# Optimization experiments

Hardware: AMD Instinct MI355X
Metric: run time of the kernel (lower is better)

## Reference

```python
import jax, jax.numpy as jnp
import numpy as np

TAU = 0.1

def setup_inputs() -> dict:
    key = jax.random.key(0)
    kZ, k1, k2 = jax.random.split(key, 3)
    N, D = 8192, 128
    scale = 1.0 / np.sqrt(D)
    return {
        "Z": jax.random.normal(kZ, (N, D), dtype=jnp.float32),
        "W1": jax.random.normal(k1, (D, D), dtype=jnp.float32) * scale,
        "b1": jnp.zeros((D,), dtype=jnp.float32),
        "W2": jax.random.normal(k2, (D, D), dtype=jnp.float32) * scale,
        "b2": jnp.zeros((D,), dtype=jnp.float32),
    }

def reference(Z, W1, b1, W2, b2):
    # DiffusivityTransform: 2-layer MLP with ReLU (torch Linear: x @ W.T + b;
    # here W1/W2 are stored already transposed as [in, out])
    t = jax.nn.relu(Z @ W1 + b1) @ W2 + b2          # [N, D]
    sim = t @ t.T                                     # [N, N]
    S = jax.nn.softmax(sim, axis=1)                   # row-stochastic [N, N]
    Z_prop = S @ Z                                    # [N, D]
    return Z + TAU * (Z_prop - Z)
```

## Files before the change

### kernel.cpp

```cpp
#include <hip/hip_runtime.h>

typedef _Float16 half_t;
typedef _Float16 hx8 __attribute__((ext_vector_type(8)));
typedef _Float16 hx4 __attribute__((ext_vector_type(4)));
typedef float fx4 __attribute__((ext_vector_type(4)));

#define LOG2E 1.44269504088896f
#define TAU 0.1f
#define NSPLIT 8

__global__ __launch_bounds__(256) void prep_kernel(
    const float* __restrict__ W1, const float* __restrict__ W2,
    const float* __restrict__ Z,
    half_t* __restrict__ W1t, half_t* __restrict__ W2t,
    half_t* __restrict__ Zth)
{
  __shared__ float tile[32*132];
  const int bx = blockIdx.x;
  const int tid = threadIdx.x;
  if (bx < 8) {
    const float* W = (bx & 4) ? W2 : W1;
    half_t* Wt = (bx & 4) ? W2t : W1t;
    const int i0 = (bx & 3) * 32;
    const int r = tid >> 3, cb = tid & 7;
#pragma unroll
    for (int it=0; it<4; ++it) {
      int c4 = cb*4 + it*32;
      *(fx4*)(&tile[r*132 + c4]) = *(const fx4*)(W + (size_t)(i0+r)*128 + c4);
    }
    __syncthreads();
    const int o = tid >> 1, ih = (tid & 1)*16;
    hx8 v0, v1;
#pragma unroll
    for (int u=0;u<8;++u) v0[u] = (half_t)tile[(ih+u)*132 + o];
#pragma unroll
    for (int u=0;u<8;++u) v1[u] = (half_t)tile[(ih+8+u)*132 + o];
    *(hx8*)(Wt + (size_t)o*128 + i0 + ih)     = v0;
    *(hx8*)(Wt + (size_t)o*128 + i0 + ih + 8) = v1;
  } else {
    float* zt = tile;
    const int b = bx - 8;
    const int nb = b >> 2;
    const int db = b & 3;
#pragma unroll
    for (int i=0;i<2;++i) {
      int fid = i*256 + tid;
      int r = fid >> 3, c4 = (fid & 7) * 4;
      *(fx4*)(&zt[r*36 + c4]) = *(const fx4*)(Z + (size_t)(nb*64 + r)*128 + db*32 + c4);
    }
    __syncthreads();
    const int cr = tid >> 3, j = tid & 7, n0 = j*8;
    hx8 hv;
#pragma unroll
    for (int idx=0;idx<8;++idx) hv[idx] = (half_t)zt[(n0+idx)*36 + cr];
    *(hx8*)(Zth + (size_t)(db*32 + cr)*8192 + nb*64 + n0) = hv;
  }
}

__global__ __launch_bounds__(128) void mlp_kernel(
    const float* __restrict__ Z, const half_t* __restrict__ W1t,
    const float* __restrict__ b1, const half_t* __restrict__ W2t,
    const float* __restrict__ b2, half_t* __restrict__ T)
{
  __shared__ half_t Hs[2][16*136];
  const int tid = threadIdx.x;
  const int w = tid >> 6, lane = tid & 63;
  const int q = lane >> 4, c = lane & 15;
  const int wrow = blockIdx.x*32 + w*16;

  hx8 zb[4];
#pragma unroll
  for (int ks=0;ks<4;++ks) {
    fx4 a = *(const fx4*)(Z + (size_t)(wrow + c)*128 + ks*32 + q*8);
    fx4 b = *(const fx4*)(Z + (size_t)(wrow + c)*128 + ks*32 + q*8 + 4);
#pragma unroll
    for (int u=0;u<4;++u) { zb[ks][u] = (half_t)a[u]; zb[ks][4+u] = (half_t)b[u]; }
  }
  fx4 acc[8];
#pragma unroll
  for (int mt=0;mt<8;++mt) acc[mt] = (fx4){0.f,0.f,0.f,0.f};
#pragma unroll
  for (int mt=0;mt<8;++mt)
#pragma unroll
    for (int ks=0;ks<4;++ks) {
      hx8 aw = *(const hx8*)(W1t + (size_t)(mt*16 + c)*128 + ks*32 + q*8);
      acc[mt] = __builtin_amdgcn_mfma_f32_16x16x32_f16(aw, zb[ks], acc[mt], 0,0,0);
    }
#pragma unroll
  for (int mt=0;mt<8;++mt) {
    fx4 bias = *(const fx4*)(b1 + mt*16 + 4*q);
    hx4 hv;
#pragma unroll
    for (int i=0;i<4;++i) {
      float h = acc[mt][i] + bias[i];
      hv[i] = (half_t)(h > 0.f ? h : 0.f);
    }
    *(hx4*)(&Hs[w][c*136 + mt*16 + 4*q]) = hv;
  }

  hx8 hb[4];
#pragma unroll
  for (int ks=0;ks<4;++ks) hb[ks] = *(const hx8*)(&Hs[w][c*136 + ks*32 + q*8]);
#pragma unroll
  for (int mt=0;mt<8;++mt) acc[mt] = (fx4){0.f,0.f,0.f,0.f};
#pragma unroll
  for (int mt=0;mt<8;++mt)
#pragma unroll
    for (int ks=0;ks<4;++ks) {
      hx8 aw = *(const hx8*)(W2t + (size_t)(mt*16 + c)*128 + ks*32 + q*8);
      acc[mt] = __builtin_amdgcn_mfma_f32_16x16x32_f16(aw, hb[ks], acc[mt], 0,0,0);
    }
#pragma unroll
  for (int mt=0;mt<8;++mt) {
    fx4 bias = *(const fx4*)(b2 + mt*16 + 4*q);
    hx4 tv;
#pragma unroll
    for (int i=0;i<4;++i) tv[i] = (half_t)(acc[mt][i] + bias[i]);
    *(hx4*)(T + (size_t)(wrow + c)*128 + mt*16 + 4*q) = tv;
  }
}

__global__ __launch_bounds__(256,2) void flash_kernel(
    const half_t* __restrict__ T, const half_t* __restrict__ Zt,
    half_t* __restrict__ Pacc, float* __restrict__ Pm, float* __restrict__ Pl)
{
  __shared__ half_t Tbuf[2][16*512];
  __shared__ half_t Zbuf[2][16*512];
  const int tid = threadIdx.x;
  const int w = tid >> 6, lane = tid & 63;
  const int q = lane >> 4, c = lane & 15;
  const int bx = blockIdx.x;
  const int qb = bx >> 3, kh = bx & 7;
  const int wrow = qb*128 + w*32;
  const int sw = (c & 7) * 8;

  hx8 bq[2][4];
#pragma unroll
  for (int nt=0;nt<2;++nt)
#pragma unroll
    for (int ks=0;ks<4;++ks)
      bq[nt][ks] = *(const hx8*)(T + (size_t)(wrow + nt*16 + c)*128 + ks*32 + q*8);

  fx4 oacc[8][2];
#pragma unroll
  for (int mtd=0;mtd<8;++mtd)
#pragma unroll
    for (int nt=0;nt<2;++nt) oacc[mtd][nt] = (fx4){0.f,0.f,0.f,0.f};
  float m_run[2] = {-1e30f,-1e30f};
  float l_run[2] = {0.f,0.f};

  const int kbase = kh*1024;

  auto issue_loads = [&](int kt0, int b) {
    if (w < 2) {
#pragma unroll
      for (int i=0;i<8;++i) {
        int f = w*8 + i, mt = f >> 2, ks = f & 3;
        const half_t* gp = T + (size_t)(kt0 + mt*16 + c)*128 + ks*32 + q*8;
        half_t* lp = &Tbuf[b][f*512 + lane*8];
        __builtin_amdgcn_global_load_lds(
            (const __attribute__((address_space(1))) void*)gp,
            (__attribute__((address_space(3))) void*)lp, 16, 0, 0);
      }
    } else {
#pragma unroll
      for (int i=0;i<8;++i) {
        int f2 = (w-2)*8 + i, mtd = f2 >> 1, ks2 = f2 & 1;
        const half_t* gp = Zt + (size_t)(mtd*16 + c)*8192 + kt0 + ks2*32 + q*8;
        half_t* lp = &Zbuf[b][f2*512 + lane*8];
        __builtin_amdgcn_global_load_lds(
            (const __attribute__((address_space(1))) void*)gp,
            (__attribute__((address_space(3))) void*)lp, 16, 0, 0);
      }
    }
  };

  issue_loads(kbase, 0);

  for (int t=0;t<16;++t) {
    const int cur = t & 1;
    __syncthreads();
    half_t* Tcur = Tbuf[cur];
    half_t* Zcur = Zbuf[cur];
    half_t* Psw  = &Tbuf[cur][w*2048];

    fx4 sacc[4][2];
#pragma unroll
    for (int mt=0;mt<4;++mt)
#pragma unroll
      for (int nt=0;nt<2;++nt) sacc[mt][nt] = (fx4){0.f,0.f,0.f,0.f};
#pragma unroll
    for (int ks=0;ks<4;++ks)
#pragma unroll
      for (int mt=0;mt<4;++mt) {
        hx8 ak = *(const hx8*)(&Tcur[(mt*4+ks)*512 + lane*8]);
        sacc[mt][0] = __builtin_amdgcn_mfma_f32_16x16x32_f16(ak, bq[0][ks], sacc[mt][0], 0,0,0);
        sacc[mt][1] = __builtin_amdgcn_mfma_f32_16x16x32_f16(ak, bq[1][ks], sacc[mt][1], 0,0,0);
      }

    hx4 pk[2][4];
#pragma unroll
    for (int nt=0;nt<2;++nt) {
      float mx = -1e30f;
#pragma unroll
      for (int mt=0;mt<4;++mt)
#pragma unroll
        for (int i=0;i<4;++i) mx = fmaxf(mx, sacc[mt][nt][i]);
      mx = fmaxf(mx, __shfl_xor(mx, 16, 64));
      mx = fmaxf(mx, __shfl_xor(mx, 32, 64));
      float mnew = fmaxf(m_run[nt], mx);
      float alpha = __builtin_amdgcn_exp2f((m_run[nt]-mnew)*LOG2E);
      m_run[nt] = mnew;
      float nb = mnew*LOG2E;
      float rs = 0.f;
#pragma unroll
      for (int mt=0;mt<4;++mt) {
#pragma unroll
        for (int i=0;i<4;++i) {
          float p = __builtin_amdgcn_exp2f(sacc[mt][nt][i]*LOG2E - nb);
          rs += p;
          pk[nt][mt][i] = (half_t)p;
        }
      }
      rs += __shfl_xor(rs, 16, 64);
      rs += __shfl_xor(rs, 32, 64);
      l_run[nt] = l_run[nt]*alpha + rs;
#pragma unroll
      for (int mtd=0;mtd<8;++mtd)
#pragma unroll
        for (int i=0;i<4;++i) oacc[mtd][nt][i] *= alpha;
    }

    __syncthreads();
    if (t < 15) issue_loads(kbase + (t+1)*64, cur ^ 1);

#pragma unroll
    for (int nt=0;nt<2;++nt)
#pragma unroll
      for (int mt=0;mt<4;++mt)
        *(hx4*)(&Psw[(nt*16 + c)*64 + ((mt*16 + 4*q) ^ sw)]) = pk[nt][mt];

#pragma unroll
    for (int ks2=0;ks2<2;++ks2) {
      hx8 bp0 = *(const hx8*)(&Psw[(c     )*64 + ((ks2*32 + q*8) ^ sw)]);
      hx8 bp1 = *(const hx8*)(&Psw[(16 + c)*64 + ((ks2*32 + q*8) ^ sw)]);
#pragma unroll
      for (int mtd=0;mtd<8;++mtd) {
        hx8 az = *(const hx8*)(&Zcur[(mtd*2+ks2)*512 + lane*8]);
        oacc[mtd][0] = __builtin_amdgcn_mfma_f32_16x16x32_f16(az, bp0, oacc[mtd][0], 0,0,0);
        oacc[mtd][1] = __builtin_amdgcn_mfma_f32_16x16x32_f16(az, bp1, oacc[mtd][1], 0,0,0);
      }
    }
  }

#pragma unroll
  for (int nt=0;nt<2;++nt) {
    float inv = 1.0f / l_run[nt];
    const size_t rowg = (size_t)(bx*128 + w*32 + nt*16 + c);
#pragma unroll
    for (int mtd=0;mtd<8;++mtd) {
      hx4 ov;
#pragma unroll
      for (int i=0;i<4;++i) ov[i] = (half_t)(oacc[mtd][nt][i]*inv);
      *(hx4*)(Pacc + rowg*128 + mtd*16 + 4*q) = ov;
    }
    if (q == 0) {
      Pm[rowg] = m_run[nt];
      Pl[rowg] = l_run[nt];
    }
  }
}

__global__ __launch_bounds__(256) void merge_kernel(
    const float* __restrict__ Z, const half_t* __restrict__ Pacc,
    const float* __restrict__ Pm, const float* __restrict__ Pl,
    float* __restrict__ out)
{
  const int th = blockIdx.x*256 + threadIdx.x;
  const int r = th >> 5, cg = th & 31;
  const int qb = r >> 7, rr = r & 127;
  float mk[NSPLIT], lk[NSPLIT];
  float M = -1e30f;
#pragma unroll
  for (int k=0;k<NSPLIT;++k) {
    int p = qb*NSPLIT + k;
    mk[k] = Pm[p*128 + rr];
    lk[k] = Pl[p*128 + rr];
    M = fmaxf(M, mk[k]);
  }
  float L = 0.f, wk[NSPLIT];
#pragma unroll
  for (int k=0;k<NSPLIT;++k) { wk[k] = lk[k]*__builtin_amdgcn_exp2f((mk[k]-M)*LOG2E); L += wk[k]; }
  float o0=0.f,o1=0.f,o2=0.f,o3=0.f;
#pragma unroll
  for (int k=0;k<NSPLIT;++k) {
    int p = qb*NSPLIT + k;
    hx4 v = *(const hx4*)(Pacc + ((size_t)p*128 + rr)*128 + cg*4);
    o0 += wk[k]*(float)v[0]; o1 += wk[k]*(float)v[1];
    o2 += wk[k]*(float)v[2]; o3 += wk[k]*(float)v[3];
  }
  float invL = 1.0f / L;
  fx4 zv = *(const fx4*)(Z + (size_t)r*128 + cg*4);
  fx4 res;
  res[0] = (1.f-TAU)*zv[0] + TAU*o0*invL;
  res[1] = (1.f-TAU)*zv[1] + TAU*o1*invL;
  res[2] = (1.f-TAU)*zv[2] + TAU*o2*invL;
  res[3] = (1.f-TAU)*zv[3] + TAU*o3*invL;
  *(fx4*)(out + (size_t)r*128 + cg*4) = res;
}

extern "C" void kernel_launch(void* const* d_in, const int* in_sizes, int n_in,
                              void* d_out, int out_size, void* d_ws, size_t ws_size,
                              hipStream_t stream) {
  const float* Z  = (const float*)d_in[0];
  const float* W1 = (const float*)d_in[1];
  const float* b1 = (const float*)d_in[2];
  const float* W2 = (const float*)d_in[3];
  const float* b2 = (const float*)d_in[4];
  float* out = (float*)d_out;

  char* ws = (char*)d_ws;
  const size_t NBLK = 64 * NSPLIT;
  half_t* Thi  = (half_t*)(ws);
  half_t* Zth  = (half_t*)(ws + (size_t)2*1024*1024);
  half_t* Pacc = (half_t*)(ws + (size_t)4*1024*1024);
  float*  Pm   = (float*)(ws + (size_t)4*1024*1024 + NBLK*128*128*2);
  float*  Pl   = Pm + NBLK*128;
  half_t* W1t  = (half_t*)(ws + (size_t)4*1024*1024 + NBLK*128*128*2 + 2*NBLK*128*4);
  half_t* W2t  = W1t + 128*128;

  hipLaunchKernelGGL(prep_kernel,  dim3(520),  dim3(256), 0, stream, W1, W2, Z, W1t, W2t, Zth);
  hipLaunchKernelGGL(mlp_kernel,   dim3(256),  dim3(128), 0, stream, Z, W1t, b1, W2t, b2, Thi);
  hipLaunchKernelGGL(flash_kernel, dim3(NBLK), dim3(256), 0, stream, Thi, Zth, Pacc, Pm, Pl);
  hipLaunchKernelGGL(merge_kernel, dim3(1024), dim3(256), 0, stream, Z, Pacc, Pm, Pl, out);
}
```

Baseline: 131.6 us.

## Fuse split-K merge into flash kernel via atomic counter and Z transpose into MLP

```diff
diff --git a/kernel.cpp b/kernel.cpp
--- a/kernel.cpp
+++ b/kernel.cpp
@@ -9,73 +9,75 @@
 #define TAU 0.1f
 #define NSPLIT 8
 
-__global__ __launch_bounds__(256) void prep_kernel(
+__global__ __launch_bounds__(256) void wtrans_kernel(
     const float* __restrict__ W1, const float* __restrict__ W2,
-    const float* __restrict__ Z,
-    half_t* __restrict__ W1t, half_t* __restrict__ W2t,
-    half_t* __restrict__ Zth)
+    half_t* __restrict__ W1t, half_t* __restrict__ W2t)
 {
   __shared__ float tile[32*132];
   const int bx = blockIdx.x;
+  const float* W = (bx & 4) ? W2 : W1;
+  half_t* Wt = (bx & 4) ? W2t : W1t;
+  const int i0 = (bx & 3) * 32;
   const int tid = threadIdx.x;
-  if (bx < 8) {
-    const float* W = (bx & 4) ? W2 : W1;
-    half_t* Wt = (bx & 4) ? W2t : W1t;
-    const int i0 = (bx & 3) * 32;
-    const int r = tid >> 3, cb = tid & 7;
-#pragma unroll
-    for (int it=0; it<4; ++it) {
-      int c4 = cb*4 + it*32;
-      *(fx4*)(&tile[r*132 + c4]) = *(const fx4*)(W + (size_t)(i0+r)*128 + c4);
-    }
-    __syncthreads();
-    const int o = tid >> 1, ih = (tid & 1)*16;
-    hx8 v0, v1;
-#pragma unroll
-    for (int u=0;u<8;++u) v0[u] = (half_t)tile[(ih+u)*132 + o];
-#pragma unroll
-    for (int u=0;u<8;++u) v1[u] = (half_t)tile[(ih+8+u)*132 + o];
-    *(hx8*)(Wt + (size_t)o*128 + i0 + ih)     = v0;
-    *(hx8*)(Wt + (size_t)o*128 + i0 + ih + 8) = v1;
-  } else {
-    float* zt = tile;
-    const int b = bx - 8;
-    const int nb = b >> 2;
-    const int db = b & 3;
-#pragma unroll
-    for (int i=0;i<2;++i) {
-      int fid = i*256 + tid;
-      int r = fid >> 3, c4 = (fid & 7) * 4;
-      *(fx4*)(&zt[r*36 + c4]) = *(const fx4*)(Z + (size_t)(nb*64 + r)*128 + db*32 + c4);
-    }
-    __syncthreads();
-    const int cr = tid >> 3, j = tid & 7, n0 = j*8;
-    hx8 hv;
-#pragma unroll
-    for (int idx=0;idx<8;++idx) hv[idx] = (half_t)zt[(n0+idx)*36 + cr];
-    *(hx8*)(Zth + (size_t)(db*32 + cr)*8192 + nb*64 + n0) = hv;
-  }
+  const int r = tid >> 3, cb = tid & 7;
+#pragma unroll
+  for (int it=0; it<4; ++it) {
+    int c4 = cb*4 + it*32;
+    *(fx4*)(&tile[r*132 + c4]) = *(const fx4*)(W + (size_t)(i0+r)*128 + c4);
+  }
+  __syncthreads();
+  const int o = tid >> 1, ih = (tid & 1)*16;
+  hx8 v0, v1;
+#pragma unroll
+  for (int u=0;u<8;++u) v0[u] = (half_t)tile[(ih+u)*132 + o];
+#pragma unroll
+  for (int u=0;u<8;++u) v1[u] = (half_t)tile[(ih+8+u)*132 + o];
+  *(hx8*)(Wt + (size_t)o*128 + i0 + ih)     = v0;
+  *(hx8*)(Wt + (size_t)o*128 + i0 + ih + 8) = v1;
 }
 
-__global__ __launch_bounds__(128) void mlp_kernel(
+__global__ __launch_bounds__(256) void mlpz_kernel(
     const float* __restrict__ Z, const half_t* __restrict__ W1t,
     const float* __restrict__ b1, const half_t* __restrict__ W2t,
-    const float* __restrict__ b2, half_t* __restrict__ T)
+    const float* __restrict__ b2, half_t* __restrict__ T,
+    half_t* __restrict__ Zth)
 {
-  __shared__ half_t Hs[2][16*136];
+  __shared__ float Ztile[64*132];
+  __shared__ half_t Hs[4][16*136];
   const int tid = threadIdx.x;
   const int w = tid >> 6, lane = tid & 63;
   const int q = lane >> 4, c = lane & 15;
-  const int wrow = blockIdx.x*32 + w*16;
+  const int rb = blockIdx.x*64;
+  const int wrow = rb + w*16;
+
+#pragma unroll
+  for (int i=0;i<8;++i) {
+    int fid = i*256 + tid;
+    int r = fid >> 5, c4 = (fid & 31)*4;
+    *(fx4*)(&Ztile[r*132 + c4]) = *(const fx4*)(Z + (size_t)(rb + r)*128 + c4);
+  }
+  __syncthreads();
+
+  {
+    const int d = tid >> 1, n0 = (tid & 1)*32;
+#pragma unroll
+    for (int i=0;i<4;++i) {
+      hx8 hv;
+#pragma unroll
+      for (int u=0;u<8;++u) hv[u] = (half_t)Ztile[(n0 + i*8 + u)*132 + d];
+      *(hx8*)(Zth + (size_t)d*8192 + rb + n0 + i*8) = hv;
+    }
+  }
 
   hx8 zb[4];
 #pragma unroll
   for (int ks=0;ks<4;++ks) {
-    fx4 a = *(const fx4*)(Z + (size_t)(wrow + c)*128 + ks*32 + q*8);
-    fx4 b = *(const fx4*)(Z + (size_t)(wrow + c)*128 + ks*32 + q*8 + 4);
+    fx4 a = *(const fx4*)(&Ztile[(w*16 + c)*132 + ks*32 + q*8]);
+    fx4 b = *(const fx4*)(&Ztile[(w*16 + c)*132 + ks*32 + q*8 + 4]);
 #pragma unroll
     for (int u=0;u<4;++u) { zb[ks][u] = (half_t)a[u]; zb[ks][4+u] = (half_t)b[u]; }
   }
+
   fx4 acc[8];
 #pragma unroll
   for (int mt=0;mt<8;++mt) acc[mt] = (fx4){0.f,0.f,0.f,0.f};
@@ -120,9 +122,10 @@
   }
 }
 
-__global__ __launch_bounds__(256,2) void flash_kernel(
+__global__ __launch_bounds__(256,2) void flashm_kernel(
     const half_t* __restrict__ T, const half_t* __restrict__ Zt,
-    half_t* __restrict__ Pacc, float* __restrict__ Pm, float* __restrict__ Pl)
+    half_t* __restrict__ Pacc, float* __restrict__ Pm, float* __restrict__ Pl,
+    const float* __restrict__ Z, float* __restrict__ out, int* __restrict__ cnt)
 {
   __shared__ half_t Tbuf[2][16*512];
   __shared__ half_t Zbuf[2][16*512];
@@ -198,6 +201,13 @@
         sacc[mt][1] = __builtin_amdgcn_mfma_f32_16x16x32_f16(ak, bq[1][ks], sacc[mt][1], 0,0,0);
       }
 
+    hx8 az[16];
+#pragma unroll
+    for (int mtd=0;mtd<8;++mtd)
+#pragma unroll
+      for (int ks2=0;ks2<2;++ks2)
+        az[mtd*2+ks2] = *(const hx8*)(&Zcur[(mtd*2+ks2)*512 + lane*8]);
+
     hx4 pk[2][4];
 #pragma unroll
     for (int nt=0;nt<2;++nt) {
@@ -246,9 +256,8 @@
       hx8 bp1 = *(const hx8*)(&Psw[(16 + c)*64 + ((ks2*32 + q*8) ^ sw)]);
 #pragma unroll
       for (int mtd=0;mtd<8;++mtd) {
-        hx8 az = *(const hx8*)(&Zcur[(mtd*2+ks2)*512 + lane*8]);
-        oacc[mtd][0] = __builtin_amdgcn_mfma_f32_16x16x32_f16(az, bp0, oacc[mtd][0], 0,0,0);
-        oacc[mtd][1] = __builtin_amdgcn_mfma_f32_16x16x32_f16(az, bp1, oacc[mtd][1], 0,0,0);
+        oacc[mtd][0] = __builtin_amdgcn_mfma_f32_16x16x32_f16(az[mtd*2+ks2], bp0, oacc[mtd][0], 0,0,0);
+        oacc[mtd][1] = __builtin_amdgcn_mfma_f32_16x16x32_f16(az[mtd*2+ks2], bp1, oacc[mtd][1], 0,0,0);
       }
     }
   }
@@ -269,44 +278,52 @@
       Pl[rowg] = l_run[nt];
     }
   }
-}
-
-__global__ __launch_bounds__(256) void merge_kernel(
-    const float* __restrict__ Z, const half_t* __restrict__ Pacc,
-    const float* __restrict__ Pm, const float* __restrict__ Pl,
-    float* __restrict__ out)
-{
-  const int th = blockIdx.x*256 + threadIdx.x;
-  const int r = th >> 5, cg = th & 31;
-  const int qb = r >> 7, rr = r & 127;
-  float mk[NSPLIT], lk[NSPLIT];
-  float M = -1e30f;
-#pragma unroll
-  for (int k=0;k<NSPLIT;++k) {
-    int p = qb*NSPLIT + k;
-    mk[k] = Pm[p*128 + rr];
-    lk[k] = Pl[p*128 + rr];
-    M = fmaxf(M, mk[k]);
-  }
-  float L = 0.f, wk[NSPLIT];
-#pragma unroll
-  for (int k=0;k<NSPLIT;++k) { wk[k] = lk[k]*__builtin_amdgcn_exp2f((mk[k]-M)*LOG2E); L += wk[k]; }
-  float o0=0.f,o1=0.f,o2=0.f,o3=0.f;
-#pragma unroll
-  for (int k=0;k<NSPLIT;++k) {
-    int p = qb*NSPLIT + k;
-    hx4 v = *(const hx4*)(Pacc + ((size_t)p*128 + rr)*128 + cg*4);
-    o0 += wk[k]*(float)v[0]; o1 += wk[k]*(float)v[1];
-    o2 += wk[k]*(float)v[2]; o3 += wk[k]*(float)v[3];
-  }
-  float invL = 1.0f / L;
-  fx4 zv = *(const fx4*)(Z + (size_t)r*128 + cg*4);
-  fx4 res;
-  res[0] = (1.f-TAU)*zv[0] + TAU*o0*invL;
-  res[1] = (1.f-TAU)*zv[1] + TAU*o1*invL;
-  res[2] = (1.f-TAU)*zv[2] + TAU*o2*invL;
-  res[3] = (1.f-TAU)*zv[3] + TAU*o3*invL;
-  *(fx4*)(out + (size_t)r*128 + cg*4) = res;
+
+  __syncthreads();
+  int* flagp = (int*)(&Tbuf[0][0]);
+  if (tid == 0) {
+    __threadfence();
+    int old = atomicAdd(cnt + qb, 1);
+    *flagp = (old == NSPLIT-1) ? 1 : 0;
+  }
+  __syncthreads();
+  if (*flagp) {
+    __threadfence();
+    const int tr = tid >> 5, cg = tid & 31;
+#pragma unroll 1
+    for (int it=0; it<16; ++it) {
+      const int rr = it*8 + tr;
+      float mk[NSPLIT], lk[NSPLIT];
+      float M = -1e30f;
+#pragma unroll
+      for (int k=0;k<NSPLIT;++k) {
+        int p = qb*NSPLIT + k;
+        mk[k] = Pm[p*128 + rr];
+        lk[k] = Pl[p*128 + rr];
+        M = fmaxf(M, mk[k]);
+      }
+      float L = 0.f, wk[NSPLIT];
+#pragma unroll
+      for (int k=0;k<NSPLIT;++k) { wk[k] = lk[k]*__builtin_amdgcn_exp2f((mk[k]-M)*LOG2E); L += wk[k]; }
+      float o0=0.f,o1=0.f,o2=0.f,o3=0.f;
+#pragma unroll
+      for (int k=0;k<NSPLIT;++k) {
+        int p = qb*NSPLIT + k;
+        hx4 v = *(const hx4*)(Pacc + ((size_t)p*128 + rr)*128 + cg*4);
+        o0 += wk[k]*(float)v[0]; o1 += wk[k]*(float)v[1];
+        o2 += wk[k]*(float)v[2]; o3 += wk[k]*(float)v[3];
+      }
+      float invL = 1.0f / L;
+      const size_t r = (size_t)qb*128 + rr;
+      fx4 zv = *(const fx4*)(Z + r*128 + cg*4);
+      fx4 res;
+      res[0] = (1.f-TAU)*zv[0] + TAU*o0*invL;
+      res[1] = (1.f-TAU)*zv[1] + TAU*o1*invL;
+      res[2] = (1.f-TAU)*zv[2] + TAU*o2*invL;
+      res[3] = (1.f-TAU)*zv[3] + TAU*o3*invL;
+      *(fx4*)(out + r*128 + cg*4) = res;
+    }
+  }
 }
 
 extern "C" void kernel_launch(void* const* d_in, const int* in_sizes, int n_in,
@@ -328,9 +345,10 @@
   float*  Pl   = Pm + NBLK*128;
   half_t* W1t  = (half_t*)(ws + (size_t)4*1024*1024 + NBLK*128*128*2 + 2*NBLK*128*4);
   half_t* W2t  = W1t + 128*128;
-
-  hipLaunchKernelGGL(prep_kernel,  dim3(520),  dim3(256), 0, stream, W1, W2, Z, W1t, W2t, Zth);
-  hipLaunchKernelGGL(mlp_kernel,   dim3(256),  dim3(128), 0, stream, Z, W1t, b1, W2t, b2, Thi);
-  hipLaunchKernelGGL(flash_kernel, dim3(NBLK), dim3(256), 0, stream, Thi, Zth, Pacc, Pm, Pl);
-  hipLaunchKernelGGL(merge_kernel, dim3(1024), dim3(256), 0, stream, Z, Pacc, Pm, Pl, out);
+  int*    cnt  = (int*)(W2t + 128*128);
+
+  hipMemsetAsync(cnt, 0, 64*sizeof(int), stream);
+  hipLaunchKernelGGL(wtrans_kernel, dim3(8),    dim3(256), 0, stream, W1, W2, W1t, W2t);
+  hipLaunchKernelGGL(mlpz_kernel,   dim3(128),  dim3(256), 0, stream, Z, W1t, b1, W2t, b2, Thi, Zth);
+  hipLaunchKernelGGL(flashm_kernel, dim3(NBLK), dim3(256), 0, stream, Thi, Zth, Pacc, Pm, Pl, Z, out, cnt);
 }
```

New measurement: 198.5 us. +50.8%, slower.
